# Kernel tuning notes

Hardware: AMD Instinct MI355X
Metric: run time of the kernel (lower is better)

The kernel has to match this reference:

```python
import jax, jax.numpy as jnp
import numpy as np

B, S, D = 2, 2048, 768
H = 12
DEPTH = D // H
DFF = 4 * D
EPS = 1e-5


def setup_inputs() -> dict:
    key = jax.random.key(0)
    ks = jax.random.split(key, 9)
    sd = 0.02
    return {
        "x": jax.random.normal(ks[0], (B, S, D), dtype=jnp.float32),
        "Wqkv": jax.random.normal(ks[1], (D, 3 * D), dtype=jnp.float32) * sd,
        "Wout": jax.random.normal(ks[2], (D, D), dtype=jnp.float32) * sd,
        "bout": jnp.zeros((D,), dtype=jnp.float32),
        "W1": jax.random.normal(ks[3], (D, DFF), dtype=jnp.float32) * sd,
        "b1": jnp.zeros((DFF,), dtype=jnp.float32),
        "W2": jax.random.normal(ks[4], (DFF, D), dtype=jnp.float32) * sd,
        "b2": jnp.zeros((D,), dtype=jnp.float32),
        "g1": jnp.ones((D,), dtype=jnp.float32),
        "be1": jnp.zeros((D,), dtype=jnp.float32),
        "g2": jnp.ones((D,), dtype=jnp.float32),
        "be2": jnp.zeros((D,), dtype=jnp.float32),
    }


def _layernorm(x, gain, bias):
    mean = jnp.mean(x, axis=-1, keepdims=True)
    var = jnp.mean(jnp.square(x - mean), axis=-1, keepdims=True)  # unbiased=False
    return gain * (x - mean) / jnp.sqrt(var + EPS) + bias


def reference(x, Wqkv, Wout, bout, W1, b1, W2, b2, g1, be1, g2, be2):
    b, s, d = x.shape
    # QKV projection (no bias), chunk into q,k,v
    qkv = jnp.einsum("bsd,de->bse", x, Wqkv)
    q, k, v = jnp.split(qkv, 3, axis=-1)
    q = q.reshape(b, s, H, DEPTH).transpose(0, 2, 1, 3)  # bhsd
    k = k.reshape(b, s, H, DEPTH).transpose(0, 2, 1, 3)
    v = v.reshape(b, s, H, DEPTH).transpose(0, 2, 1, 3)
    scores = jnp.einsum("bhqd,bhkd->bhqk", q, k) / np.sqrt(DEPTH).astype(np.float32)
    # causal mask (use_masking=True)
    causal = jnp.tril(jnp.ones((s, s), dtype=bool))
    scores = jnp.where(causal, scores, -jnp.inf)
    attn = jax.nn.softmax(scores, axis=-1)
    ctx = jnp.einsum("bhqk,bhkd->bhqd", attn, v)
    ctx = ctx.transpose(0, 2, 1, 3).reshape(b, s, d)
    attn_out = jnp.einsum("bsd,de->bse", ctx, Wout) + bout
    # residual + LN1 (dropout is identity in eval)
    h = _layernorm(x + attn_out, g1, be1)
    # FFN
    ff = jax.nn.relu(jnp.einsum("bsd,df->bsf", h, W1) + b1)
    ff = jnp.einsum("bsf,fd->bsd", ff, W2) + b2
    return _layernorm(h + ff, g2, be2)
```

## Files before the change

kernel.cpp:

```cpp
#include <hip/hip_runtime.h>


typedef __attribute__((ext_vector_type(8)))  short    short8;
typedef __attribute__((ext_vector_type(4)))  float    floatx4;
typedef __attribute__((ext_vector_type(16))) float    floatx16;
typedef __attribute__((ext_vector_type(4)))  unsigned uint4v;

#define QSC 0.18033688f
#define C2  24.0f

__device__ __forceinline__ float b2f(unsigned short u) {
    return __uint_as_float(((unsigned)u) << 16);
}
__device__ __forceinline__ unsigned short f2b(float f) {
    unsigned x = __float_as_uint(f);
    return (unsigned short)((x + 0x7fffu + ((x >> 16) & 1u)) >> 16);
}
__device__ __forceinline__ void async_cp16(const void* g, void* l) {
    __builtin_amdgcn_global_load_lds((const __attribute__((address_space(1))) void*)g,
                                     (__attribute__((address_space(3))) void*)l,
                                     16, 0, 0);
}
__device__ __forceinline__ unsigned cvtpk(float lo, float hi) {
    unsigned r;
    asm("v_cvt_pk_bf16_f32 %0, %1, %2" : "=v"(r) : "v"(lo), "v"(hi));
    return r;
}
__device__ __forceinline__ void plswap(unsigned& a, unsigned& b) {
    asm("v_permlane32_swap_b32 %0, %1" : "+v"(a), "+v"(b));
}
__device__ __forceinline__ int chunk_ofs8(int qb) {
    int t = qb >> 2, rem = qb & 3;
    return (t + 1) * (2 * t + rem);
}
__device__ __forceinline__ int swz16(int row, int chunk) {
    return row * 64 + (((chunk ^ (row & 7)) & 7) << 3);
}
__device__ __forceinline__ int swzB(int row, int chunk) {
    return row * 64 + (((chunk ^ (row & 7) ^ ((row >> 2) & 6)) & 7) << 3);
}

__global__ __launch_bounds__(256) void prep_all(
    const float* __restrict__ x,    unsigned short* __restrict__ xb,
    const float* __restrict__ Wqkv, unsigned short* __restrict__ wqkvT,
    const float* __restrict__ Wout, unsigned short* __restrict__ woutT,
    const float* __restrict__ W1,   unsigned short* __restrict__ w1T,
    const float* __restrict__ W2,   unsigned short* __restrict__ w2T)
{
    __shared__ float tile[32][33];
    int idx = blockIdx.x;
    int tx = threadIdx.x & 31, ty = threadIdx.x >> 5;
    if (idx >= 6912) {
        int i = (idx - 6912) * 256 + threadIdx.x;
        float4 v = ((const float4*)x)[i];
        ushort4 u;
        u.x = f2b(v.x); u.y = f2b(v.y); u.z = f2b(v.z); u.w = f2b(v.w);
        ((ushort4*)xb)[i] = u;
        return;
    }
    const float* W; unsigned short* Wt; int K, N, bx, by;
    if (idx < 1728)      { W = Wqkv; Wt = wqkvT; K = 768;  N = 2304; bx = idx % 72;        by = idx / 72; }
    else if (idx < 2304) { W = Wout; Wt = woutT; K = 768;  N = 768;  bx = (idx-1728) % 24; by = (idx-1728) / 24; }
    else if (idx < 4608) { W = W1;   Wt = w1T;   K = 768;  N = 3072; bx = (idx-2304) % 96; by = (idx-2304) / 96; }
    else                 { W = W2;   Wt = w2T;   K = 3072; N = 768;  bx = (idx-4608) % 24; by = (idx-4608) / 24; }
    int n0 = bx * 32, k0 = by * 32;
    for (int i = ty; i < 32; i += 8)
        tile[i][tx] = W[(size_t)(k0 + i) * N + n0 + tx];
    __syncthreads();
    for (int i = ty; i < 32; i += 8)
        Wt[(size_t)(n0 + i) * K + k0 + tx] = f2b(tile[tx][i]);
}

__global__ __launch_bounds__(256) void gemm_bf16(
    const unsigned short* __restrict__ A,
    const unsigned short* __restrict__ Bt,
    const float* __restrict__ bias,
    float* __restrict__ outF,
    unsigned short* __restrict__ outB,
    int M, int N, int K, int relu, int mode, int kslab)
{
    __shared__ unsigned short As[2][8192];
    __shared__ unsigned short Bs[2][8192];
    const int tid  = threadIdx.x;
    const int gx   = gridDim.x;
    const int nwg  = gx * gridDim.y;
    const int orig = blockIdx.y * gx + blockIdx.x;
    const int qch  = nwg >> 3, rem = nwg & 7;
    const int xcd  = orig & 7, sub = orig >> 3;
    const int nid  = (xcd < rem ? xcd * (qch + 1)
                                : rem * (qch + 1) + (xcd - rem) * qch) + sub;
    const int m0   = (nid / gx) * 128;
    const int n0   = (nid % gx) * 128;
    const int kz   = blockIdx.z;
    const int kbeg = kz * kslab;
    const int kend = kbeg + kslab;
    const int lane = tid & 63;
    const int wave = tid >> 6;
    const int wm   = (wave >> 1) * 64;
    const int wn   = (wave & 1) * 64;
    const int fr   = lane & 15;
    const int fq   = lane >> 4;

    floatx4 acc[4][4];
    for (int i = 0; i < 4; i++)
        for (int j = 0; j < 4; j++)
            for (int e = 0; e < 4; e++) acc[i][j][e] = 0.f;

#define STAGE(BUF, KK)                                                         \
    {                                                                          \
        _Pragma("unroll")                                                      \
        for (int r_ = 0; r_ < 4; ++r_) {                                       \
            int c_   = r_ * 256 + tid;       \
            int row_ = c_ >> 3;                                                \
            int jj_  = ((c_ & 7) ^ (row_ & 7)) * 8;  \
            async_cp16(A  + (size_t)(m0 + row_) * K + (KK) + jj_, &As[BUF][c_ * 8]); \
            async_cp16(Bt + (size_t)(n0 + row_) * K + (KK) + jj_, &Bs[BUF][c_ * 8]); \
        }                                                                      \
    }

    STAGE(0, kbeg);
    __syncthreads();
    int cur = 0;
    for (int kk = kbeg; kk < kend; kk += 64) {
        if (kk + 64 < kend) STAGE(cur ^ 1, kk + 64);
        #pragma unroll
        for (int kc = 0; kc < 2; ++kc) {
            short8 a[4], b[4];
            #pragma unroll
            for (int t = 0; t < 4; t++) a[t] = *(const short8*)&As[cur][swz16(wm + t * 16 + fr, kc * 4 + fq)];
            #pragma unroll
            for (int t = 0; t < 4; t++) b[t] = *(const short8*)&Bs[cur][swz16(wn + t * 16 + fr, kc * 4 + fq)];
            #pragma unroll
            for (int i = 0; i < 4; i++)
                #pragma unroll
                for (int j = 0; j < 4; j++)
                    acc[i][j] = __builtin_amdgcn_mfma_f32_16x16x32_bf16(a[i], b[j], acc[i][j], 0, 0, 0);
        }
        __syncthreads();
        cur ^= 1;
    }
#undef STAGE

    if (mode == 2) {
        float* dst = outF + (size_t)kz * M * N;
        #pragma unroll
        for (int j = 0; j < 4; j++) {
            int col = n0 + wn + j * 16 + fr;
            #pragma unroll
            for (int i = 0; i < 4; i++) {
                int rbase = m0 + wm + i * 16 + fq * 4;
                #pragma unroll
                for (int e = 0; e < 4; e++)
                    dst[(size_t)(rbase + e) * N + col] = acc[i][j][e];
            }
        }
        return;
    }
    if (mode == 1) {
        #pragma unroll
        for (int j = 0; j < 4; j++) {
            int col   = n0 + wn + j * 16 + fr;
            int which = (col >= 1536) ? 2 : (col >= 768 ? 1 : 0);
            float sc  = (which == 0) ? QSC : 1.0f;
            int rem_  = col - which * 768;
            int hh    = rem_ >> 6, d = rem_ & 63;
            #pragma unroll
            for (int i = 0; i < 4; i++) {
                int rbase = m0 + wm + i * 16 + fq * 4;
                #pragma unroll
                for (int e = 0; e < 4; e++) {
                    int row = rbase + e;
                    int b_  = row >> 11, srow = row & 2047;
                    size_t idx = (size_t)which * 3145728 +
                                 ((size_t)(b_ * 12 + hh) * 2048 + srow) * 64 + d;
                    outB[idx] = f2b(acc[i][j][e] * sc);
                }
            }
        }
        return;
    }
    #pragma unroll
    for (int j = 0; j < 4; j++) {
        int col  = n0 + wn + j * 16 + fr;
        float bv = bias ? bias[col] : 0.f;
        #pragma unroll
        for (int i = 0; i < 4; i++) {
            int rbase = m0 + wm + i * 16 + fq * 4;
            #pragma unroll
            for (int e = 0; e < 4; e++) {
                float v = acc[i][j][e] + bv;
                if (relu) v = fmaxf(v, 0.f);
                size_t idx = (size_t)(rbase + e) * N + col;
                if (outF) outF[idx] = v;
                if (outB) outB[idx] = f2b(v);
            }
        }
    }
}

__global__ __launch_bounds__(256, 4) void attn_part(const unsigned short* __restrict__ Qg,
                                                    const unsigned short* __restrict__ Kg,
                                                    const unsigned short* __restrict__ Vg,
                                                    unsigned short* __restrict__ pO,
                                                    float* __restrict__ pL) {
    __shared__ unsigned short Ks[2][4096];
    __shared__ unsigned short Vt[2][4096];
    const int tid  = threadIdx.x;
    const int lane = tid & 63;
    const int wave = tid >> 6;
    const int ql   = lane & 31;
    const int hi   = lane >> 5;
    const int wm   = wave * 32;
    const int bid  = blockIdx.y * 40 + blockIdx.x;
    const int swz  = (bid & 7) * 120 + (bid >> 3);
    const int bh   = swz / 40;
    const int r    = 39 - (swz % 40);
    int qb = 0;
    for (int q_ = 15; q_ >= 0; --q_) if (r >= chunk_ofs8(q_)) { qb = q_; break; }
    const int c     = r - chunk_ofs8(qb);
    const int q0    = qb * 128;
    const int tile0 = 8 * c;
    const int ntk   = min(8, 2 * (qb + 1) - 8 * c);
    const int slot  = bh * 40 + r;
    const unsigned short* Qb = Qg + (size_t)bh * 131072;
    const unsigned short* Kb = Kg + (size_t)bh * 131072;
    const unsigned short* Vb = Vg + (size_t)bh * 131072;
    const int qrow = q0 + wm + ql;

    short8 qf[4];
    {
        const unsigned short* qr = Qb + (size_t)qrow * 64 + hi * 8;
        #pragma unroll
        for (int c4 = 0; c4 < 4; ++c4)
            qf[c4] = *(const short8*)(qr + c4 * 16);
    }

    floatx16 o[2];
    #pragma unroll
    for (int db = 0; db < 2; ++db)
        #pragma unroll
        for (int e = 0; e < 16; ++e) o[db][e] = 0.f;
    float ls[4] = {0.f, 0.f, 0.f, 0.f};

    const int c0 = tid, c1 = tid + 256;
    uint4 kr0, kr1, vr0, vr1;

#define LOADT(TG)                                                              \
    {                                                                          \
        int base = (TG) * 64;                                                  \
        kr0 = *(const uint4*)(Kb + (size_t)(base + (c0 >> 3)) * 64 + (c0 & 7) * 8); \
        kr1 = *(const uint4*)(Kb + (size_t)(base + (c1 >> 3)) * 64 + (c1 & 7) * 8); \
        vr0 = *(const uint4*)(Vb + (size_t)(base + (c0 & 63)) * 64 + (c0 >> 6) * 8); \
        vr1 = *(const uint4*)(Vb + (size_t)(base + (c1 & 63)) * 64 + (c1 >> 6) * 8); \
    }
#define WRITET(BUF)                                                            \
    {                                                                          \
        *(uint4*)&Ks[BUF][swzB(c0 >> 3, c0 & 7)] = kr0;                       \
        *(uint4*)&Ks[BUF][swzB(c1 >> 3, c1 & 7)] = kr1;                       \
        unsigned short t0[8]; *(uint4*)t0 = vr0;                               \
        _Pragma("unroll") for (int i_ = 0; i_ < 8; ++i_) {                     \
            int rv = (c0 >> 6) * 8 + i_;                                       \
            Vt[BUF][rv * 64 + (((((c0 >> 3) & 7) ^ i_ ^ ((rv >> 2) & 6)) & 7) << 3) + (c0 & 7)] = t0[i_]; \
        }                                                                      \
        unsigned short t1[8]; *(uint4*)t1 = vr1;                               \
        _Pragma("unroll") for (int i_ = 0; i_ < 8; ++i_) {                     \
            int rv = (c1 >> 6) * 8 + i_;                                       \
            Vt[BUF][rv * 64 + (((((c1 >> 3) & 7) ^ i_ ^ ((rv >> 2) & 6)) & 7) << 3) + (c1 & 7)] = t1[i_]; \
        }                                                                      \
    }

    LOADT(tile0);
    WRITET(0);
    __syncthreads();

    for (int kt = 0; kt < ntk; ++kt) {
        const int  tg   = tile0 + kt;
        const int  cur  = kt & 1;
        const bool more = (kt + 1 < ntk);
        if (more) LOADT(tg + 1);

        #pragma unroll
        for (int bb = 0; bb < 2; ++bb) {
            short8 kf[4];
            #pragma unroll
            for (int c4 = 0; c4 < 4; ++c4)
                kf[c4] = *(const short8*)&Ks[cur][swzB(32 * bb + ql, 2 * c4 + hi)];
            floatx16 s;
            #pragma unroll
            for (int e = 0; e < 16; ++e) s[e] = 0.f;
            #pragma unroll
            for (int c4 = 0; c4 < 4; ++c4)
                s = __builtin_amdgcn_mfma_f32_32x32x16_bf16(kf[c4], qf[c4], s, 0, 0, 0);

            const int  kvb = tg * 64 + 32 * bb + 4 * hi;
            const bool nm  = (tg * 64 + 32 * bb + 31) > (q0 + wm);
            if (nm) {
                #pragma unroll
                for (int e = 0; e < 16; ++e)
                    if (kvb + (e & 3) + 8 * (e >> 2) > qrow) s[e] = -1e30f;
            }
            float pv[16];
            #pragma unroll
            for (int e = 0; e < 16; ++e) {
                pv[e] = __builtin_amdgcn_exp2f(s[e] - C2);
                ls[e & 3] += pv[e];
            }

            unsigned w[8];
            #pragma unroll
            for (int m = 0; m < 4; ++m) {
                w[2 * m]     = cvtpk(pv[4 * m],     pv[4 * m + 1]);
                w[2 * m + 1] = cvtpk(pv[4 * m + 2], pv[4 * m + 3]);
            }
            plswap(w[0], w[2]);
            plswap(w[1], w[3]);
            plswap(w[4], w[6]);
            plswap(w[5], w[7]);
            uint4v u0 = {w[0], w[1], w[2], w[3]};
            uint4v u1 = {w[4], w[5], w[6], w[7]};
            short8 pa0 = __builtin_bit_cast(short8, u0);
            short8 pa1 = __builtin_bit_cast(short8, u1);

            #pragma unroll
            for (int db = 0; db < 2; ++db) {
                short8 vf0 = *(const short8*)&Vt[cur][swzB(32 * db + ql, 4 * bb + hi)];
                short8 vf1 = *(const short8*)&Vt[cur][swzB(32 * db + ql, 4 * bb + 2 + hi)];
                o[db] = __builtin_amdgcn_mfma_f32_32x32x16_bf16(pa0, vf0, o[db], 0, 0, 0);
                o[db] = __builtin_amdgcn_mfma_f32_32x32x16_bf16(pa1, vf1, o[db], 0, 0, 0);
            }
        }

        if (more) {
            WRITET(cur ^ 1);
            __syncthreads();
        }
    }
#undef LOADT
#undef WRITET

    float lsum = (ls[0] + ls[1]) + (ls[2] + ls[3]);
    lsum += __shfl_xor(lsum, 32);

    __syncthreads();
    unsigned short* Ost = &Ks[0][0];
    #pragma unroll
    for (int db = 0; db < 2; ++db)
        #pragma unroll
        for (int e = 0; e < 16; ++e) {
            int row = wm + (e & 3) + 8 * (e >> 2) + 4 * hi;
            int col = db * 32 + ql;
            Ost[row * 64 + ((((col >> 3) ^ (row & 7)) & 7) << 3) + (col & 7)] =
                f2b(o[db][e]);
        }
    __syncthreads();
    #pragma unroll
    for (int p = 0; p < 4; ++p) {
        int chunk = p * 256 + tid;
        int row = chunk >> 3, cc = chunk & 7;
        uint4 val = *(const uint4*)&Ost[row * 64 + (((cc ^ (row & 7)) & 7) << 3)];
        *(uint4*)(pO + ((size_t)slot * 128 + row) * 64 + cc * 8) = val;
    }
    if (lane < 32)
        pL[(size_t)slot * 128 + wm + ql] = lsum;
}

__global__ __launch_bounds__(256) void attn_combine(const unsigned short* __restrict__ pO,
                                                    const float* __restrict__ pL,
                                                    unsigned short* __restrict__ ctx) {
    const int qb  = blockIdx.x;
    const int bh  = blockIdx.y;
    const int b   = bh / 12, h = bh % 12;
    const int nch = (qb >> 2) + 1;
    const int slot0 = bh * 40 + chunk_ofs8(qb);
    const int tid = threadIdx.x;
    const int row = tid >> 1;
    const int col0 = (tid & 1) * 32;

    float L = 0.f;
    for (int i = 0; i < nch; ++i)
        L += pL[(size_t)(slot0 + i) * 128 + row];

    float acc[32];
    #pragma unroll
    for (int j = 0; j < 32; ++j) acc[j] = 0.f;
    for (int i = 0; i < nch; ++i) {
        const unsigned short* p = pO + ((size_t)(slot0 + i) * 128 + row) * 64 + col0;
        #pragma unroll
        for (int v4 = 0; v4 < 4; ++v4) {
            uint4 u = *(const uint4*)(p + v4 * 8);
            unsigned short t[8]; *(uint4*)t = u;
            #pragma unroll
            for (int j = 0; j < 8; ++j) acc[v4 * 8 + j] += b2f(t[j]);
        }
    }
    float inv = 1.f / L;
    unsigned short* orow = ctx + ((size_t)(b * 2048 + qb * 128 + row)) * 768 + h * 64 + col0;
    #pragma unroll
    for (int v4 = 0; v4 < 4; ++v4) {
        unsigned short t[8];
        #pragma unroll
        for (int j = 0; j < 8; ++j) t[j] = f2b(acc[v4 * 8 + j] * inv);
        *(uint4*)(orow + v4 * 8) = *(uint4*)t;
    }
}

__global__ __launch_bounds__(256) void resid_ln2(const float* __restrict__ X,
                                                 const float* __restrict__ P,
                                                 int nsplit,
                                                 const float* __restrict__ bv,
                                                 const float* __restrict__ gain,
                                                 const float* __restrict__ beta,
                                                 float* __restrict__ outF,
                                                 unsigned short* __restrict__ outB) {
    const int row = blockIdx.x;
    const int t   = threadIdx.x;
    const size_t off = (size_t)row * 768;
    float v[3];
    #pragma unroll
    for (int i = 0; i < 3; i++) {
        size_t c = off + t + i * 256;
        float r = X[c] + bv[t + i * 256];
        for (int p = 0; p < nsplit; ++p) r += P[(size_t)p * 3145728 + c];
        v[i] = r;
    }
    float s  = v[0] + v[1] + v[2];
    float s2 = v[0] * v[0] + v[1] * v[1] + v[2] * v[2];
    #pragma unroll
    for (int o2 = 32; o2 > 0; o2 >>= 1) {
        s  += __shfl_down(s,  o2);
        s2 += __shfl_down(s2, o2);
    }
    __shared__ float rs[4], rq[4];
    if ((t & 63) == 0) { rs[t >> 6] = s; rq[t >> 6] = s2; }
    __syncthreads();
    float S    = rs[0] + rs[1] + rs[2] + rs[3];
    float S2   = rq[0] + rq[1] + rq[2] + rq[3];
    float mean = S * (1.0f / 768.0f);
    float var  = S2 * (1.0f / 768.0f) - mean * mean;
    float inv  = rsqrtf(var + 1e-5f);
    #pragma unroll
    for (int i = 0; i < 3; i++) {
        int c   = t + i * 256;
        float y = gain[c] * (v[i] - mean) * inv + beta[c];
        if (outF) outF[off + c] = y;
        if (outB) outB[off + c] = f2b(y);
    }
}

extern "C" void kernel_launch(void* const* d_in, const int* in_sizes, int n_in,
                              void* d_out, int out_size, void* d_ws, size_t ws_size,
                              hipStream_t stream) {
    const float* x    = (const float*)d_in[0];
    const float* Wqkv = (const float*)d_in[1];
    const float* Wout = (const float*)d_in[2];
    const float* bout = (const float*)d_in[3];
    const float* W1   = (const float*)d_in[4];
    const float* b1   = (const float*)d_in[5];
    const float* W2   = (const float*)d_in[6];
    const float* b2   = (const float*)d_in[7];
    const float* g1   = (const float*)d_in[8];
    const float* be1  = (const float*)d_in[9];
    const float* g2   = (const float*)d_in[10];
    const float* be2  = (const float*)d_in[11];
    float* out = (float*)d_out;

    char* ws = (char*)d_ws;
    unsigned short* wqkvT  = (unsigned short*)(ws + 0);
    unsigned short* woutT  = (unsigned short*)(ws + 3538944);
    unsigned short* w1T    = (unsigned short*)(ws + 4718592);
    unsigned short* w2T    = (unsigned short*)(ws + 9437184);
    unsigned short* xb     = (unsigned short*)(ws + 14155776);
    unsigned short* qkvG   = (unsigned short*)(ws + 20447232);
    unsigned short* Qg     = qkvG;
    unsigned short* Kg     = qkvG + 3145728;
    unsigned short* Vg     = qkvG + 6291456;
    unsigned short* pO     = (unsigned short*)(ws + 39321600);
    float*          pL     = (float*)(ws + 67633152);
    unsigned short* ctxb   = (unsigned short*)(ws + 14155776);
    float*          WoutP  = (float*)(ws + 39321600);
    float*          h      = (float*)(ws + 20447232);
    unsigned short* hb     = (unsigned short*)(ws + 77070336);
    unsigned short* ffb    = (unsigned short*)(ws + 39321600);
    float*          W2P    = (float*)(ws + 64487424);

    prep_all<<<9984, 256, 0, stream>>>(x, xb, Wqkv, wqkvT, Wout, woutT, W1, w1T, W2, w2T);
    gemm_bf16<<<dim3(18, 32), 256, 0, stream>>>(xb, wqkvT, nullptr, nullptr, qkvG,
                                                4096, 2304, 768, 0, 1, 768);
    attn_part<<<dim3(40, 24), 256, 0, stream>>>(Qg, Kg, Vg, pO, pL);
    attn_combine<<<dim3(16, 24), 256, 0, stream>>>(pO, pL, ctxb);
    gemm_bf16<<<dim3(6, 32, 3), 256, 0, stream>>>(ctxb, woutT, nullptr, WoutP, nullptr,
                                                  4096, 768, 768, 0, 2, 256);
    resid_ln2<<<4096, 256, 0, stream>>>(x, WoutP, 3, bout, g1, be1, h, hb);
    gemm_bf16<<<dim3(24, 32), 256, 0, stream>>>(hb, w1T, b1, nullptr, ffb,
                                                4096, 3072, 768, 1, 0, 768);
    gemm_bf16<<<dim3(6, 32, 2), 256, 0, stream>>>(ffb, w2T, nullptr, W2P, nullptr,
                                                  4096, 768, 3072, 0, 2, 1536);
    resid_ln2<<<4096, 256, 0, stream>>>(h, W2P, 2, b2, g2, be2, out, nullptr);
}
```

Measured before the change: 302.2 us.

## Split causal attention into 4-tile KV chunks and raise MFMA priority

Halves the KV chunk length per attention block from 8 to 4 tiles, so the grid grows from 40 to 72 blocks per head. This is meant to balance work better across CUs and shorten the tail of the causal triangle. The slot offsets and chunk counts in the combine kernel are updated to match. It also wraps the MFMA groups in s_setprio, hoists the V fragment LDS reads ahead of the PV MFMAs, and moves the partial row-sum store earlier. The trade-off is more partial outputs written and then read back by the combine kernel.

```diff
diff --git a/kernel.cpp b/kernel.cpp
--- a/kernel.cpp
+++ b/kernel.cpp
@@ -29,9 +29,9 @@
 __device__ __forceinline__ void plswap(unsigned& a, unsigned& b) {
     asm("v_permlane32_swap_b32 %0, %1" : "+v"(a), "+v"(b));
 }
-__device__ __forceinline__ int chunk_ofs8(int qb) {
-    int t = qb >> 2, rem = qb & 3;
-    return (t + 1) * (2 * t + rem);
+__device__ __forceinline__ int chunk_ofs4(int qb) {
+    int t = qb >> 1;
+    return (qb & 1) ? (t + 1) * (t + 1) : t * (t + 1);
 }
 __device__ __forceinline__ int swz16(int row, int chunk) {
     return row * 64 + (((chunk ^ (row & 7)) & 7) << 3);
@@ -211,17 +211,17 @@
     const int ql   = lane & 31;
     const int hi   = lane >> 5;
     const int wm   = wave * 32;
-    const int bid  = blockIdx.y * 40 + blockIdx.x;
-    const int swz  = (bid & 7) * 120 + (bid >> 3);
-    const int bh   = swz / 40;
-    const int r    = 39 - (swz % 40);
+    const int bid  = blockIdx.y * 72 + blockIdx.x;
+    const int swz  = (bid & 7) * 216 + (bid >> 3);
+    const int bh   = swz / 72;
+    const int r    = 71 - (swz % 72);
     int qb = 0;
-    for (int q_ = 15; q_ >= 0; --q_) if (r >= chunk_ofs8(q_)) { qb = q_; break; }
-    const int c     = r - chunk_ofs8(qb);
+    for (int q_ = 15; q_ >= 0; --q_) if (r >= chunk_ofs4(q_)) { qb = q_; break; }
+    const int c     = r - chunk_ofs4(qb);
     const int q0    = qb * 128;
-    const int tile0 = 8 * c;
-    const int ntk   = min(8, 2 * (qb + 1) - 8 * c);
-    const int slot  = bh * 40 + r;
+    const int tile0 = 4 * c;
+    const int ntk   = min(4, 2 * (qb + 1) - 4 * c);
+    const int slot  = bh * 72 + r;
     const unsigned short* Qb = Qg + (size_t)bh * 131072;
     const unsigned short* Kb = Kg + (size_t)bh * 131072;
     const unsigned short* Vb = Vg + (size_t)bh * 131072;
@@ -288,9 +288,11 @@
             floatx16 s;
             #pragma unroll
             for (int e = 0; e < 16; ++e) s[e] = 0.f;
+            __builtin_amdgcn_s_setprio(1);
             #pragma unroll
             for (int c4 = 0; c4 < 4; ++c4)
                 s = __builtin_amdgcn_mfma_f32_32x32x16_bf16(kf[c4], qf[c4], s, 0, 0, 0);
+            __builtin_amdgcn_s_setprio(0);
 
             const int  kvb = tg * 64 + 32 * bb + 4 * hi;
             const bool nm  = (tg * 64 + 32 * bb + 31) > (q0 + wm);
@@ -321,13 +323,19 @@
             short8 pa0 = __builtin_bit_cast(short8, u0);
             short8 pa1 = __builtin_bit_cast(short8, u1);
 
+            short8 vf[2][2];
             #pragma unroll
             for (int db = 0; db < 2; ++db) {
-                short8 vf0 = *(const short8*)&Vt[cur][swzB(32 * db + ql, 4 * bb + hi)];
-                short8 vf1 = *(const short8*)&Vt[cur][swzB(32 * db + ql, 4 * bb + 2 + hi)];
-                o[db] = __builtin_amdgcn_mfma_f32_32x32x16_bf16(pa0, vf0, o[db], 0, 0, 0);
-                o[db] = __builtin_amdgcn_mfma_f32_32x32x16_bf16(pa1, vf1, o[db], 0, 0, 0);
-            }
+                vf[db][0] = *(const short8*)&Vt[cur][swzB(32 * db + ql, 4 * bb + hi)];
+                vf[db][1] = *(const short8*)&Vt[cur][swzB(32 * db + ql, 4 * bb + 2 + hi)];
+            }
+            __builtin_amdgcn_s_setprio(1);
+            #pragma unroll
+            for (int db = 0; db < 2; ++db) {
+                o[db] = __builtin_amdgcn_mfma_f32_32x32x16_bf16(pa0, vf[db][0], o[db], 0, 0, 0);
+                o[db] = __builtin_amdgcn_mfma_f32_32x32x16_bf16(pa1, vf[db][1], o[db], 0, 0, 0);
+            }
+            __builtin_amdgcn_s_setprio(0);
         }
 
         if (more) {
@@ -340,6 +348,8 @@
 
     float lsum = (ls[0] + ls[1]) + (ls[2] + ls[3]);
     lsum += __shfl_xor(lsum, 32);
+    if (lane < 32)
+        pL[(size_t)slot * 128 + wm + ql] = lsum;
 
     __syncthreads();
     unsigned short* Ost = &Ks[0][0];
@@ -360,8 +370,6 @@
         uint4 val = *(const uint4*)&Ost[row * 64 + (((cc ^ (row & 7)) & 7) << 3)];
         *(uint4*)(pO + ((size_t)slot * 128 + row) * 64 + cc * 8) = val;
     }
-    if (lane < 32)
-        pL[(size_t)slot * 128 + wm + ql] = lsum;
 }
 
 __global__ __launch_bounds__(256) void attn_combine(const unsigned short* __restrict__ pO,
@@ -370,8 +378,8 @@
     const int qb  = blockIdx.x;
     const int bh  = blockIdx.y;
     const int b   = bh / 12, h = bh % 12;
-    const int nch = (qb >> 2) + 1;
-    const int slot0 = bh * 40 + chunk_ofs8(qb);
+    const int nch = (qb + 2) >> 1;
+    const int slot0 = bh * 72 + chunk_ofs4(qb);
     const int tid = threadIdx.x;
     const int row = tid >> 1;
     const int col0 = (tid & 1) * 32;
@@ -486,7 +494,7 @@
     prep_all<<<9984, 256, 0, stream>>>(x, xb, Wqkv, wqkvT, Wout, woutT, W1, w1T, W2, w2T);
     gemm_bf16<<<dim3(18, 32), 256, 0, stream>>>(xb, wqkvT, nullptr, nullptr, qkvG,
                                                 4096, 2304, 768, 0, 1, 768);
-    attn_part<<<dim3(40, 24), 256, 0, stream>>>(Qg, Kg, Vg, pO, pL);
+    attn_part<<<dim3(72, 24), 256, 0, stream>>>(Qg, Kg, Vg, pO, pL);
     attn_combine<<<dim3(16, 24), 256, 0, stream>>>(pO, pL, ctxb);
     gemm_bf16<<<dim3(6, 32, 3), 256, 0, stream>>>(ctxb, woutT, nullptr, WoutP, nullptr,
                                                   4096, 768, 768, 0, 2, 256);
```

New measurement: 325.6 us. +7.7%, slower.
